# Optimization experiments

Measured on AMD Instinct MI355X. Metric: run time of the kernel, lower is better.

## Reference

```python
import jax, jax.numpy as jnp
import numpy as np
import math

B, R, C = 4, 512, 512
E, H, D, M, F = 256, 16, 16, 16, 512  # embed, heads, qkv_dim, ms_hidden, ff_hidden
EPS = 1e-5


def setup_inputs() -> dict:
    key = jax.random.key(0)
    ks = jax.random.split(key, 20)
    s = lambda fan_in: 1.0 / math.sqrt(fan_in)
    u = lambda k, shape, lim: jax.random.uniform(k, shape, jnp.float32, -lim, lim)
    mix1_init = (1 / 2) ** 0.5
    mix2_init = (1 / 16) ** 0.5
    return {
        "row_emb": jax.random.normal(ks[0], (B, R, E), jnp.float32),
        "col_emb": jax.random.normal(ks[1], (B, C, E), jnp.float32),
        "cost_mat": jax.random.uniform(ks[2], (B, R, C), jnp.float32),
        "Wq": u(ks[3], (E, H * D), s(E)),
        "Wk": u(ks[4], (E, H * D), s(E)),
        "Wv": u(ks[5], (E, H * D), s(E)),
        "mix1_w": u(ks[6], (H, 2, M), mix1_init),
        "mix1_b": u(ks[7], (H, M), mix1_init),
        "mix2_w": u(ks[8], (H, M, 1), mix2_init),
        "mix2_b": u(ks[9], (H, 1), mix2_init),
        "Wc": u(ks[10], (H * D, E), s(H * D)),
        "bc": u(ks[11], (E,), s(H * D)),
        "W1": u(ks[12], (E, F), s(E)),
        "b1": u(ks[13], (F,), s(E)),
        "W2": u(ks[14], (F, E), s(F)),
        "b2": u(ks[15], (E,), s(F)),
        "g1": jnp.ones((E,), jnp.float32),
        "be1": jnp.zeros((E,), jnp.float32),
        "g2": jnp.ones((E,), jnp.float32),
        "be2": jnp.zeros((E,), jnp.float32),
    }


def _instance_norm(x, gamma, beta):
    # InstanceNorm1d on x permuted to (B, E, L): normalize over seq dim per (b, channel)
    mean = jnp.mean(x, axis=1, keepdims=True)          # [B,1,E]
    var = jnp.mean((x - mean) ** 2, axis=1, keepdims=True)
    return (x - mean) * jax.lax.rsqrt(var + EPS) * gamma + beta


def reference(row_emb, col_emb, cost_mat, Wq, Wk, Wv, mix1_w, mix1_b, mix2_w,
              mix2_b, Wc, bc, W1, b1, W2, b2, g1, be1, g2, be2):
    # QKV projections, split heads: [B,L,H*D] -> [B,H,L,D]
    q = (row_emb @ Wq).reshape(B, R, H, D).transpose(0, 2, 1, 3)
    k = (col_emb @ Wk).reshape(B, C, H, D).transpose(0, 2, 1, 3)
    v = (col_emb @ Wv).reshape(B, C, H, D).transpose(0, 2, 1, 3)

    dot = jnp.einsum('bhrd,bhcd->bhrc', q, k) / math.sqrt(D)
    cost = jnp.broadcast_to(cost_mat[:, None, :, :], (B, H, R, C))
    two = jnp.stack((dot, cost), axis=-1)               # [B,H,R,C,2]

    # per-head 2 -> M -> 1 mixing MLP over scores
    ms1 = jnp.einsum('bhrcs,hsm->bhrcm', two, mix1_w) + mix1_b[None, :, None, None, :]
    ms1 = jax.nn.relu(ms1)
    mixed = jnp.einsum('bhrcm,hm->bhrc', ms1, mix2_w[:, :, 0]) + mix2_b[:, 0][None, :, None, None]

    weights = jax.nn.softmax(mixed, axis=-1)            # [B,H,R,C]
    out = jnp.einsum('bhrc,bhcd->bhrd', weights, v)
    out_concat = out.transpose(0, 2, 1, 3).reshape(B, R, H * D)

    mh = out_concat @ Wc + bc                           # multi_head_combine

    # TransformerFFN with instance norm
    x = _instance_norm(row_emb + mh, g1, be1)
    ffn = jax.nn.relu(x @ W1 + b1) @ W2 + b2
    return _instance_norm(x + ffn, g2, be2)
```

## Files before the change

### kernel.cpp

```cpp
#include <hip/hip_runtime.h>
#include <hip/hip_bf16.h>

typedef __hip_bfloat16 bf16;
typedef __hip_bfloat162 bf162;
typedef _Float16 f16;
typedef __attribute__((ext_vector_type(2))) _Float16 h2;
typedef __attribute__((ext_vector_type(8))) short short8;
typedef __attribute__((ext_vector_type(4))) float f32x4;
typedef __attribute__((ext_vector_type(2))) float f32x2;

#define B_ 4
#define R_ 512
#define C_ 512
#define E_ 256
#define H_ 16
#define D_ 16

__device__ __forceinline__ float b2f(bf16 x) { return __bfloat162float(x); }
__device__ __forceinline__ void stout(bf16* p, float v) { *p = __float2bfloat16(v); }
__device__ __forceinline__ void stout(f16* p, float v) { *p = (f16)v; }

__global__ __launch_bounds__(256) void transpose_cvt_kernel(
    const float* __restrict__ Wq, const float* __restrict__ Wk, const float* __restrict__ Wv,
    const float* __restrict__ Wc, const float* __restrict__ W1, const float* __restrict__ W2,
    bf16* __restrict__ WqT, bf16* __restrict__ WkT, bf16* __restrict__ WvT,
    bf16* __restrict__ WcT, bf16* __restrict__ W1T, bf16* __restrict__ W2T,
    float* __restrict__ statsZ)
{
    __shared__ bf16 tile[32][33];
    const int wsel = blockIdx.y;
    const int tx = blockIdx.x;
    if (wsel == 0 && tx >= 64) {
        const int idx = (tx - 64) * 256 + threadIdx.x;
        if (idx < 4096) statsZ[idx] = 0.f;
        return;
    }
    const float* src; bf16* dst; int K, N; float scl = 1.0f;
    switch (wsel) {
        case 0: src = Wq; dst = WqT; K = 256; N = 256; scl = 0.25f; break;
        case 1: src = Wk; dst = WkT; K = 256; N = 256; break;
        case 2: src = Wv; dst = WvT; K = 256; N = 256; break;
        case 3: src = Wc; dst = WcT; K = 256; N = 256; break;
        case 4: src = W1; dst = W1T; K = 256; N = 512; break;
        default: src = W2; dst = W2T; K = 512; N = 256; break;
    }
    const int ntiles = (K >> 5) * (N >> 5);
    if (tx >= ntiles) return;
    const int ncnt = N >> 5;
    const int tk = tx / ncnt, tn = tx % ncnt;
    const int c = threadIdx.x & 31, r = threadIdx.x >> 5;
#pragma unroll
    for (int i = 0; i < 4; i++)
        tile[r + i * 8][c] = __float2bfloat16(scl * src[(size_t)(tk * 32 + r + i * 8) * N + tn * 32 + c]);
    __syncthreads();
#pragma unroll
    for (int i = 0; i < 4; i++)
        dst[(size_t)(tn * 32 + r + i * 8) * K + tk * 32 + c] = tile[c][r + i * 8];
}

template <int AMODE, typename OT, int BM, int BN, bool BIAS, int RES, bool RELU, bool STATS>
__device__ __forceinline__ void mfma_gemm_body(
    const void* __restrict__ Ap,
    const bf16* __restrict__ BT, const float* __restrict__ bias,
    const void* __restrict__ Res,
    const float* __restrict__ normS, const float* __restrict__ normG, const float* __restrict__ normB,
    float* __restrict__ statsOut, OT* __restrict__ Cout,
    int M, int N, int K, int bx, int by)
{
    constexpr int MT = BM / 32, NT = BN / 32;
    constexpr int AEL = BM * 64 / 256, BEL = BN * 64 / 256;
    __shared__ __align__(16) bf16 As[BM * 80];
    __shared__ __align__(16) bf16 Bs[BN * 80];
    const int tid = threadIdx.x;
    const int wid = tid >> 6, lane = tid & 63;
    const int wm = wid >> 1, wn = wid & 1;
    const int fr = lane & 15, quad = lane >> 4;
    const int m0 = by * BM, n0 = bx * BN;
    const int arow = (AEL == 16) ? (tid >> 2) : (tid >> 3);
    const int akg  = (AEL == 16) ? ((tid & 3) << 4) : ((tid & 7) << 3);
    const int brow = (BEL == 16) ? (tid >> 2) : (tid >> 3);
    const int bkg  = (BEL == 16) ? ((tid & 3) << 4) : ((tid & 7) << 3);

    f32x4 acc[MT][NT];
#pragma unroll
    for (int mt = 0; mt < MT; mt++)
#pragma unroll
        for (int nt = 0; nt < NT; nt++) acc[mt][nt] = (f32x4){0.f, 0.f, 0.f, 0.f};

    for (int k0 = 0; k0 < K; k0 += 64) {
        if constexpr (AMODE == 0) {
            const short8* gp = (const short8*)((const bf16*)Ap + (size_t)(m0 + arow) * K + k0 + akg);
#pragma unroll
            for (int t8 = 0; t8 < AEL / 8; t8++) *(short8*)(&As[arow * 80 + akg + 8 * t8]) = gp[t8];
        } else if constexpr (AMODE == 1) {
            const float4* gp = (const float4*)((const float*)Ap + (size_t)(m0 + arow) * K + k0 + akg);
#pragma unroll
            for (int j = 0; j < AEL / 4; j++) {
                const float4 f = gp[j];
                *(bf162*)(&As[arow * 80 + akg + j * 4])     = __float22bfloat162_rn(make_float2(f.x, f.y));
                *(bf162*)(&As[arow * 80 + akg + j * 4 + 2]) = __float22bfloat162_rn(make_float2(f.z, f.w));
            }
        } else {
            const int bb = (m0 + arow) >> 9;
            const bf16* ap = (const bf16*)Ap + (size_t)(m0 + arow) * K + k0 + akg;
            bf16 tmp[AEL];
#pragma unroll
            for (int t8 = 0; t8 < AEL / 8; t8++) *(short8*)(tmp + 8 * t8) = ((const short8*)ap)[t8];
#pragma unroll
            for (int j = 0; j < AEL; j++) {
                const int e = k0 + akg + j;
                const float s = normS[bb * 256 + e], sq = normS[1024 + bb * 256 + e];
                const float mn = s * (1.f / 512.f);
                float var = sq * (1.f / 512.f) - mn * mn; var = fmaxf(var, 0.f);
                As[arow * 80 + akg + j] = __float2bfloat16(
                    (b2f(tmp[j]) - mn) * rsqrtf(var + 1e-5f) * normG[e] + normB[e]);
            }
        }
        {
            const short8* gp = (const short8*)(BT + (size_t)(n0 + brow) * K + k0 + bkg);
#pragma unroll
            for (int t8 = 0; t8 < BEL / 8; t8++) *(short8*)(&Bs[brow * 80 + bkg + 8 * t8]) = gp[t8];
        }
        __syncthreads();

        short8 af[MT][2], bfr[NT][2];
#pragma unroll
        for (int mt = 0; mt < MT; mt++) {
            const int ar = wm * (BM / 2) + mt * 16 + fr;
#pragma unroll
            for (int kh = 0; kh < 2; kh++)
                af[mt][kh] = *(const short8*)(&As[ar * 80 + quad * 8 + kh * 32]);
        }
#pragma unroll
        for (int nt = 0; nt < NT; nt++) {
            const int br = wn * (BN / 2) + nt * 16 + fr;
#pragma unroll
            for (int kh = 0; kh < 2; kh++)
                bfr[nt][kh] = *(const short8*)(&Bs[br * 80 + quad * 8 + kh * 32]);
        }
#pragma unroll
        for (int kh = 0; kh < 2; kh++)
#pragma unroll
            for (int mt = 0; mt < MT; mt++)
#pragma unroll
                for (int nt = 0; nt < NT; nt++)
                    acc[mt][nt] = __builtin_amdgcn_mfma_f32_16x16x32_bf16(
                        af[mt][kh], bfr[nt][kh], acc[mt][nt], 0, 0, 0);
        __syncthreads();
    }

    float vsum[NT], vss[NT];
#pragma unroll
    for (int nt = 0; nt < NT; nt++) { vsum[nt] = 0.f; vss[nt] = 0.f; }
#pragma unroll
    for (int mt = 0; mt < MT; mt++) {
#pragma unroll
        for (int nt = 0; nt < NT; nt++) {
#pragma unroll
            for (int i = 0; i < 4; i++) {
                const int row = m0 + wm * (BM / 2) + mt * 16 + quad * 4 + i;
                const int col = n0 + wn * (BN / 2) + nt * 16 + fr;
                float v = acc[mt][nt][i];
                if (BIAS) v += bias[col];
                if constexpr (RES == 1) v += ((const float*)Res)[(size_t)row * N + col];
                if constexpr (RES == 3) {
                    const int bb = row >> 9;
                    const float yv = b2f(((const bf16*)Res)[(size_t)row * N + col]);
                    const float s = normS[bb * 256 + col], sq = normS[1024 + bb * 256 + col];
                    const float mn = s * (1.f / 512.f);
                    float var = sq * (1.f / 512.f) - mn * mn; var = fmaxf(var, 0.f);
                    v += (yv - mn) * rsqrtf(var + 1e-5f) * normG[col] + normB[col];
                }
                if (RELU) v = fmaxf(v, 0.f);
                stout(&Cout[(size_t)row * N + col], v);
                if (STATS) { vsum[nt] += v; vss[nt] += v * v; }
            }
        }
    }
    if constexpr (STATS) {
        float* sred = (float*)As;
#pragma unroll
        for (int nt = 0; nt < NT; nt++) {
            float a = vsum[nt]; a += __shfl_xor(a, 16, 64); a += __shfl_xor(a, 32, 64);
            float c = vss[nt];  c += __shfl_xor(c, 16, 64); c += __shfl_xor(c, 32, 64);
            if (quad == 0) {
                const int cl = wn * (BN / 2) + nt * 16 + fr;
                sred[wm * (2 * BN) + cl * 2 + 0] = a;
                sred[wm * (2 * BN) + cl * 2 + 1] = c;
            }
        }
        __syncthreads();
        if (tid < 2 * BN) {
            const int cl = tid >> 1, w = tid & 1;
            const float tot = sred[cl * 2 + w] + sred[2 * BN + cl * 2 + w];
            atomicAdd(&statsOut[w * 1024 + (m0 >> 9) * 256 + n0 + cl], tot);
        }
    }
}

template <int AMODE, typename OT, int BM, int BN, bool BIAS, int RES, bool RELU, bool STATS>
__global__ __launch_bounds__(256) void mfma_gemm_kernel(
    const void* __restrict__ Ap,
    const bf16* __restrict__ BT, const float* __restrict__ bias,
    const void* __restrict__ Res,
    const float* __restrict__ normS, const float* __restrict__ normG, const float* __restrict__ normB,
    float* __restrict__ statsOut, OT* __restrict__ Cout, int M, int N, int K)
{
    mfma_gemm_body<AMODE, OT, BM, BN, BIAS, RES, RELU, STATS>(
        Ap, BT, bias, Res, normS, normG, normB, statsOut, Cout,
        M, N, K, blockIdx.x, blockIdx.y);
}

__global__ __launch_bounds__(256) void qkv_kernel(
    const float* __restrict__ rowE, const float* __restrict__ colE,
    const bf16* __restrict__ WqT, const bf16* __restrict__ WkT, const bf16* __restrict__ WvT,
    f16* __restrict__ qo, f16* __restrict__ ko, f16* __restrict__ vo)
{
    const int z = blockIdx.z;
    const float* A = (z == 0) ? rowE : colE;
    const bf16* BT = (z == 0) ? WqT : (z == 1) ? WkT : WvT;
    f16* O = (z == 0) ? qo : (z == 1) ? ko : vo;
    mfma_gemm_body<1, f16, 32, 64, false, 0, false, false>(
        A, BT, nullptr, nullptr, nullptr, nullptr, nullptr, nullptr, O,
        2048, 256, 256, blockIdx.x, blockIdx.y);
}

__global__ __launch_bounds__(256) void attn_kernel(
    const f16* __restrict__ q, const f16* __restrict__ k, const f16* __restrict__ v,
    const float* __restrict__ cost, const float* __restrict__ m1w, const float* __restrict__ m1b,
    const float* __restrict__ m2w, const float* __restrict__ m2b,
    bf16* __restrict__ po, bf16* __restrict__ plb)
{
    __shared__ __align__(16) char slds[12288];
    f16* kbuf = (f16*)slds;
    float* vbuf = (float*)(slds + 4096);
    f16* smo = (f16*)slds;
    float* sml = (float*)(slds + 8192);

    const int rt = blockIdx.x >> 2, cs = blockIdx.x & 3;
    const int h = blockIdx.y, b = blockIdx.z;
    const int tid = threadIdx.x, wid = tid >> 6, lane = tid & 63;

    {
        const size_t base = ((size_t)b * C_) * 256 + h * 16 + (size_t)cs * 128 * 256;
        const int lc = tid >> 1, dp = (tid & 1) * 8;
        const size_t g = base + (size_t)lc * 256 + dp;
        *(short8*)(&kbuf[lc * 16 + dp]) = *(const short8*)(k + g);
        const short8 vraw = *(const short8*)(v + g);
        const h2* rh = (const h2*)&vraw;
        *(float4*)(&vbuf[lc * 16 + dp]) = make_float4(
            (float)rh[0].x, (float)rh[0].y, (float)rh[1].x, (float)rh[1].y);
        *(float4*)(&vbuf[lc * 16 + dp + 4]) = make_float4(
            (float)rh[2].x, (float)rh[2].y, (float)rh[3].x, (float)rh[3].y);
    }

    h2 w1a2[8], w1b2[8], b1h[8], w2p[8];
#pragma unroll
    for (int i = 0; i < 8; i++) {
        h2 t;
        t.x = (f16)m1w[h * 32 + 2 * i];      t.y = (f16)m1w[h * 32 + 2 * i + 1];      w1a2[i] = t;
        t.x = (f16)m1w[h * 32 + 16 + 2 * i]; t.y = (f16)m1w[h * 32 + 17 + 2 * i];     w1b2[i] = t;
        t.x = (f16)m1b[h * 16 + 2 * i];      t.y = (f16)m1b[h * 16 + 2 * i + 1];      b1h[i] = t;
        t.x = (f16)m2w[h * 16 + 2 * i];      t.y = (f16)m2w[h * 16 + 2 * i + 1];      w2p[i] = t;
    }
    const float b2v = m2b[h];
    const h2 zero2 = (h2)(f16)0;

    const int r = rt * 64 + lane;
    short8 qraw[2];
    {
        const short8* qp = (const short8*)(q + (size_t)(b * R_ + r) * 256 + h * 16);
        qraw[0] = qp[0]; qraw[1] = qp[1];
    }
    const h2* qh = (const h2*)qraw;

    __syncthreads();

    const float* crow = cost + (size_t)(b * R_ + r) * C_ + cs * 128 + wid * 32;
    float lrun = 0.f;
    f32x2 o2[8];
#pragma unroll
    for (int j = 0; j < 8; j++) o2[j] = (f32x2){0.f, 0.f};

    for (int cc = 0; cc < 32; cc += 4) {
        const float4 cst4 = *(const float4*)(crow + cc);
#pragma unroll
        for (int u = 0; u < 4; u++) {
            const int lc = wid * 32 + cc + u;
            const h2* kr = (const h2*)(&kbuf[lc * 16]);
            h2 dacc = qh[0] * kr[0];
#pragma unroll
            for (int i = 1; i < 8; i++) dacc = qh[i] * kr[i] + dacc;
            const float dot = (float)dacc.x + (float)dacc.y;
            const float cst = (u == 0) ? cst4.x : (u == 1) ? cst4.y : (u == 2) ? cst4.z : cst4.w;
            const f16 doth = (f16)dot, csth = (f16)cst;
            h2 dot2; dot2.x = doth; dot2.y = doth;
            h2 cst2; cst2.x = csth; cst2.y = csth;
            h2 acc2 = (h2)(f16)0;
#pragma unroll
            for (int i = 0; i < 8; i++) {
                h2 t = dot2 * w1a2[i] + b1h[i];
                t = cst2 * w1b2[i] + t;
                t = __builtin_elementwise_max(t, zero2);
                acc2 = t * w2p[i] + acc2;
            }
            const float p = __expf(b2v + (float)acc2.x + (float)acc2.y);
            lrun += p;
            f32x2 p2; p2.x = p; p2.y = p;
            const f32x2* vr = (const f32x2*)(&vbuf[lc * 16]);
#pragma unroll
            for (int j = 0; j < 8; j++) o2[j] = p2 * vr[j] + o2[j];
        }
    }

    __syncthreads();
    {
        const float invw = 1.f / lrun;
        h2* op = (h2*)&smo[(wid * 64 + lane) * 16];
#pragma unroll
        for (int j = 0; j < 8; j++) {
            h2 t; t.x = (f16)(o2[j].x * invw); t.y = (f16)(o2[j].y * invw);
            op[j] = t;
        }
        sml[wid * 64 + lane] = lrun;
    }
    __syncthreads();

    if (tid < 64) {
        const int rr = tid;
        float ll = 0.f, oo[16] = {};
#pragma unroll
        for (int w = 0; w < 4; w++) {
            const float lw = sml[w * 64 + rr];
            ll += lw;
            const h2* p = (const h2*)&smo[(w * 64 + rr) * 16];
#pragma unroll
            for (int j = 0; j < 8; j++) {
                const h2 t = p[j];
                oo[2 * j]     = fmaf(lw, (float)t.x, oo[2 * j]);
                oo[2 * j + 1] = fmaf(lw, (float)t.y, oo[2 * j + 1]);
            }
        }
        const float inv = 1.f / ll;
        const int idx = ((b * H_ + h) << 9) + rt * 64 + rr;
        plb[cs * 32768 + idx] = __float2bfloat16(ll);
        bf162* pp = (bf162*)(po + (size_t)(cs * 32768 + idx) * 16);
#pragma unroll
        for (int j = 0; j < 8; j++)
            pp[j] = __float22bfloat162_rn(make_float2(oo[2 * j] * inv, oo[2 * j + 1] * inv));
    }
}

__global__ __launch_bounds__(256) void attn_merge_kernel(
    const bf16* __restrict__ po, const bf16* __restrict__ plb, bf16* __restrict__ sa)
{
    const int idx = blockIdx.x * 256 + threadIdx.x;
    const float l0 = b2f(plb[idx]), l1 = b2f(plb[32768 + idx]);
    const float l2 = b2f(plb[65536 + idx]), l3 = b2f(plb[98304 + idx]);
    const float inv = 1.f / (l0 + l1 + l2 + l3);
    float oo[16] = {};
#pragma unroll
    for (int c = 0; c < 4; c++) {
        const float wgt = ((c == 0) ? l0 : (c == 1) ? l1 : (c == 2) ? l2 : l3) * inv;
        const bf162* pp = (const bf162*)(po + (size_t)(c * 32768 + idx) * 16);
#pragma unroll
        for (int j = 0; j < 8; j++) {
            const float2 f = __bfloat1622float2(pp[j]);
            oo[2 * j]     = fmaf(wgt, f.x, oo[2 * j]);
            oo[2 * j + 1] = fmaf(wgt, f.y, oo[2 * j + 1]);
        }
    }
    const int b = idx >> 13, h = (idx >> 9) & 15, r = idx & 511;
    bf162* dst = (bf162*)(sa + (size_t)(b * R_ + r) * 256 + h * 16);
#pragma unroll
    for (int j = 0; j < 8; j++)
        dst[j] = __float22bfloat162_rn(make_float2(oo[2 * j], oo[2 * j + 1]));
}

__global__ __launch_bounds__(256) void apply_in2_kernel(
    const bf16* __restrict__ xin, const float* __restrict__ stats,
    const float* __restrict__ g, const float* __restrict__ be, float* __restrict__ outp)
{
    const int base = (blockIdx.x * 256 + threadIdx.x) * 4;
    const int b = base >> 17;
    const bf162* xp = (const bf162*)(xin + base);
    const float2 x0 = __bfloat1622float2(xp[0]), x1 = __bfloat1622float2(xp[1]);
    const float xv[4] = {x0.x, x0.y, x1.x, x1.y};
    float4 rr;
    float* rp = (float*)&rr;
#pragma unroll
    for (int j = 0; j < 4; j++) {
        const int e = (base & 255) + j;
        const float s = stats[b * 256 + e], sq = stats[1024 + b * 256 + e];
        const float mn = s * (1.f / 512.f);
        float var = sq * (1.f / 512.f) - mn * mn; var = fmaxf(var, 0.f);
        rp[j] = (xv[j] - mn) * rsqrtf(var + 1e-5f) * g[e] + be[e];
    }
    *(float4*)(outp + base) = rr;
}

extern "C" void kernel_launch(void* const* d_in, const int* in_sizes, int n_in,
                              void* d_out, int out_size, void* d_ws, size_t ws_size,
                              hipStream_t stream)
{
    (void)in_sizes; (void)n_in; (void)out_size; (void)ws_size;
    const float* row_emb = (const float*)d_in[0];
    const float* col_emb = (const float*)d_in[1];
    const float* cost    = (const float*)d_in[2];
    const float* Wq  = (const float*)d_in[3];
    const float* Wk  = (const float*)d_in[4];
    const float* Wv  = (const float*)d_in[5];
    const float* m1w = (const float*)d_in[6];
    const float* m1b = (const float*)d_in[7];
    const float* m2w = (const float*)d_in[8];
    const float* m2b = (const float*)d_in[9];
    const float* Wc  = (const float*)d_in[10];
    const float* bc  = (const float*)d_in[11];
    const float* W1  = (const float*)d_in[12];
    const float* b1  = (const float*)d_in[13];
    const float* W2  = (const float*)d_in[14];
    const float* b2  = (const float*)d_in[15];
    const float* g1  = (const float*)d_in[16];
    const float* be1 = (const float*)d_in[17];
    const float* g2  = (const float*)d_in[18];
    const float* be2 = (const float*)d_in[19];
    float* out = (float*)d_out;

    char* w = (char*)d_ws;
    f16*  sq  = (f16*)(w + 0);
    f16*  sk  = (f16*)(w + 1048576);
    f16*  sv  = (f16*)(w + 2097152);
    bf16* sa  = (bf16*)(w + 0);
    bf16* sy  = (bf16*)(w + 1048576);
    bf16* st  = (bf16*)(w + 2097152);
    bf16* WqT = (bf16*)(w + 3145728);
    bf16* WkT = WqT + 65536;
    bf16* WvT = WkT + 65536;
    bf16* po  = (bf16*)(w + 3145728);
    bf16* shm = (bf16*)(w + 3145728);
    bf16* plb = (bf16*)(w + 7340032);
    bf16* WcT = (bf16*)(w + 7602176);
    bf16* W1T = (bf16*)(w + 7733248);
    bf16* W2T = (bf16*)(w + 7995392);
    float* stats1 = (float*)(w + 8257536);
    float* stats2 = stats1 + 2048;

    const dim3 blk(256);

    transpose_cvt_kernel<<<dim3(128, 6), blk, 0, stream>>>(
        Wq, Wk, Wv, Wc, W1, W2, WqT, WkT, WvT, WcT, W1T, W2T, stats1);

    qkv_kernel<<<dim3(4, 64, 3), blk, 0, stream>>>(row_emb, col_emb, WqT, WkT, WvT, sq, sk, sv);

    attn_kernel<<<dim3(32, 16, 4), blk, 0, stream>>>(
        sq, sk, sv, cost, m1w, m1b, m2w, m2b, po, plb);

    attn_merge_kernel<<<dim3(128), blk, 0, stream>>>(po, plb, sa);

    mfma_gemm_kernel<0, bf16, 32, 32, true, 1, false, true><<<dim3(8, 64), blk, 0, stream>>>(
        sa, WcT, bc, row_emb, nullptr, nullptr, nullptr, stats1, sy, 2048, 256, 256);

    mfma_gemm_kernel<2, bf16, 32, 64, true, 0, true, false><<<dim3(8, 64), blk, 0, stream>>>(
        sy, W1T, b1, nullptr, stats1, g1, be1, nullptr, shm, 2048, 512, 256);

    mfma_gemm_kernel<0, bf16, 32, 32, true, 3, false, true><<<dim3(8, 64), blk, 0, stream>>>(
        shm, W2T, b2, sy, stats1, g1, be1, stats2, st, 2048, 256, 512);

    apply_in2_kernel<<<dim3(512), blk, 0, stream>>>(st, stats2, g2, be2, out);
}
```

Measured before the change: 163.9 us.

## Use MFMA for attention PV, drop weight transpose kernel, read fp32 weights directly

The attention kernel now computes the mixing-MLP scores per lane for 16 rows per wave. It does an in-register max-subtracted softmax and accumulates P·V with a bf16 16x16x32 MFMA instead of scalar FMAs and an LDS cross-wave merge. V is stored as bf16 and the partial sums are kept in fp32. The separate weight transpose/convert kernel is removed: GEMMs load fp32 weights column-wise from global memory and convert on the fly, and stats zeroing moves into the merge kernel. This saves a launch and the scalar PV work, but the B-tile loads become strided, uncoalesced scalar reads.

After: 175.2 us. +6.9%, slower.

```diff
diff --git a/kernel.cpp b/kernel.cpp
--- a/kernel.cpp
+++ b/kernel.cpp
@@ -7,7 +7,6 @@
 typedef __attribute__((ext_vector_type(2))) _Float16 h2;
 typedef __attribute__((ext_vector_type(8))) short short8;
 typedef __attribute__((ext_vector_type(4))) float f32x4;
-typedef __attribute__((ext_vector_type(2))) float f32x2;
 
 #define B_ 4
 #define R_ 512
@@ -20,49 +19,10 @@
 __device__ __forceinline__ void stout(bf16* p, float v) { *p = __float2bfloat16(v); }
 __device__ __forceinline__ void stout(f16* p, float v) { *p = (f16)v; }
 
-__global__ __launch_bounds__(256) void transpose_cvt_kernel(
-    const float* __restrict__ Wq, const float* __restrict__ Wk, const float* __restrict__ Wv,
-    const float* __restrict__ Wc, const float* __restrict__ W1, const float* __restrict__ W2,
-    bf16* __restrict__ WqT, bf16* __restrict__ WkT, bf16* __restrict__ WvT,
-    bf16* __restrict__ WcT, bf16* __restrict__ W1T, bf16* __restrict__ W2T,
-    float* __restrict__ statsZ)
-{
-    __shared__ bf16 tile[32][33];
-    const int wsel = blockIdx.y;
-    const int tx = blockIdx.x;
-    if (wsel == 0 && tx >= 64) {
-        const int idx = (tx - 64) * 256 + threadIdx.x;
-        if (idx < 4096) statsZ[idx] = 0.f;
-        return;
-    }
-    const float* src; bf16* dst; int K, N; float scl = 1.0f;
-    switch (wsel) {
-        case 0: src = Wq; dst = WqT; K = 256; N = 256; scl = 0.25f; break;
-        case 1: src = Wk; dst = WkT; K = 256; N = 256; break;
-        case 2: src = Wv; dst = WvT; K = 256; N = 256; break;
-        case 3: src = Wc; dst = WcT; K = 256; N = 256; break;
-        case 4: src = W1; dst = W1T; K = 256; N = 512; break;
-        default: src = W2; dst = W2T; K = 512; N = 256; break;
-    }
-    const int ntiles = (K >> 5) * (N >> 5);
-    if (tx >= ntiles) return;
-    const int ncnt = N >> 5;
-    const int tk = tx / ncnt, tn = tx % ncnt;
-    const int c = threadIdx.x & 31, r = threadIdx.x >> 5;
-#pragma unroll
-    for (int i = 0; i < 4; i++)
-        tile[r + i * 8][c] = __float2bfloat16(scl * src[(size_t)(tk * 32 + r + i * 8) * N + tn * 32 + c]);
-    __syncthreads();
-#pragma unroll
-    for (int i = 0; i < 4; i++)
-        dst[(size_t)(tn * 32 + r + i * 8) * K + tk * 32 + c] = tile[c][r + i * 8];
-}
-
 template <int AMODE, typename OT, int BM, int BN, bool BIAS, int RES, bool RELU, bool STATS>
 __device__ __forceinline__ void mfma_gemm_body(
-    const void* __restrict__ Ap,
-    const bf16* __restrict__ BT, const float* __restrict__ bias,
-    const void* __restrict__ Res,
+    const void* __restrict__ Ap, const float* __restrict__ W, float bscl,
+    const float* __restrict__ bias, const void* __restrict__ Res,
     const float* __restrict__ normS, const float* __restrict__ normG, const float* __restrict__ normB,
     float* __restrict__ statsOut, OT* __restrict__ Cout,
     int M, int N, int K, int bx, int by)
@@ -117,9 +77,10 @@
             }
         }
         {
-            const short8* gp = (const short8*)(BT + (size_t)(n0 + brow) * K + k0 + bkg);
-#pragma unroll
-            for (int t8 = 0; t8 < BEL / 8; t8++) *(short8*)(&Bs[brow * 80 + bkg + 8 * t8]) = gp[t8];
+#pragma unroll
+            for (int j = 0; j < BEL; j++)
+                Bs[brow * 80 + bkg + j] = __float2bfloat16(
+                    bscl * W[(size_t)(k0 + bkg + j) * N + (n0 + brow)]);
         }
         __syncthreads();
 
@@ -200,58 +161,54 @@
 
 template <int AMODE, typename OT, int BM, int BN, bool BIAS, int RES, bool RELU, bool STATS>
 __global__ __launch_bounds__(256) void mfma_gemm_kernel(
-    const void* __restrict__ Ap,
-    const bf16* __restrict__ BT, const float* __restrict__ bias,
-    const void* __restrict__ Res,
+    const void* __restrict__ Ap, const float* __restrict__ W, float bscl,
+    const float* __restrict__ bias, const void* __restrict__ Res,
     const float* __restrict__ normS, const float* __restrict__ normG, const float* __restrict__ normB,
     float* __restrict__ statsOut, OT* __restrict__ Cout, int M, int N, int K)
 {
     mfma_gemm_body<AMODE, OT, BM, BN, BIAS, RES, RELU, STATS>(
-        Ap, BT, bias, Res, normS, normG, normB, statsOut, Cout,
+        Ap, W, bscl, bias, Res, normS, normG, normB, statsOut, Cout,
         M, N, K, blockIdx.x, blockIdx.y);
 }
 
 __global__ __launch_bounds__(256) void qkv_kernel(
     const float* __restrict__ rowE, const float* __restrict__ colE,
-    const bf16* __restrict__ WqT, const bf16* __restrict__ WkT, const bf16* __restrict__ WvT,
-    f16* __restrict__ qo, f16* __restrict__ ko, f16* __restrict__ vo)
+    const float* __restrict__ Wq, const float* __restrict__ Wk, const float* __restrict__ Wv,
+    f16* __restrict__ qo, f16* __restrict__ ko, bf16* __restrict__ vo)
 {
     const int z = blockIdx.z;
-    const float* A = (z == 0) ? rowE : colE;
-    const bf16* BT = (z == 0) ? WqT : (z == 1) ? WkT : WvT;
-    f16* O = (z == 0) ? qo : (z == 1) ? ko : vo;
-    mfma_gemm_body<1, f16, 32, 64, false, 0, false, false>(
-        A, BT, nullptr, nullptr, nullptr, nullptr, nullptr, nullptr, O,
-        2048, 256, 256, blockIdx.x, blockIdx.y);
+    if (z == 2) {
+        mfma_gemm_body<1, bf16, 32, 64, false, 0, false, false>(
+            colE, Wv, 1.f, nullptr, nullptr, nullptr, nullptr, nullptr, nullptr, vo,
+            2048, 256, 256, blockIdx.x, blockIdx.y);
+    } else {
+        mfma_gemm_body<1, f16, 32, 64, false, 0, false, false>(
+            (z == 0) ? rowE : colE, (z == 0) ? Wq : Wk, (z == 0) ? 0.25f : 1.f,
+            nullptr, nullptr, nullptr, nullptr, nullptr, nullptr, (z == 0) ? qo : ko,
+            2048, 256, 256, blockIdx.x, blockIdx.y);
+    }
 }
 
 __global__ __launch_bounds__(256) void attn_kernel(
-    const f16* __restrict__ q, const f16* __restrict__ k, const f16* __restrict__ v,
+    const f16* __restrict__ q, const f16* __restrict__ k, const bf16* __restrict__ v,
     const float* __restrict__ cost, const float* __restrict__ m1w, const float* __restrict__ m1b,
     const float* __restrict__ m2w, const float* __restrict__ m2b,
-    bf16* __restrict__ po, bf16* __restrict__ plb)
-{
-    __shared__ __align__(16) char slds[12288];
-    f16* kbuf = (f16*)slds;
-    float* vbuf = (float*)(slds + 4096);
-    f16* smo = (f16*)slds;
-    float* sml = (float*)(slds + 8192);
+    bf16* __restrict__ po, float* __restrict__ plf)
+{
+    __shared__ __align__(16) f16 kbuf[128 * 16];
+    __shared__ __align__(16) short vbuf[128 * 16];
 
     const int rt = blockIdx.x >> 2, cs = blockIdx.x & 3;
     const int h = blockIdx.y, b = blockIdx.z;
     const int tid = threadIdx.x, wid = tid >> 6, lane = tid & 63;
+    const int quad = lane >> 4, fr = lane & 15;
 
     {
         const size_t base = ((size_t)b * C_) * 256 + h * 16 + (size_t)cs * 128 * 256;
         const int lc = tid >> 1, dp = (tid & 1) * 8;
         const size_t g = base + (size_t)lc * 256 + dp;
         *(short8*)(&kbuf[lc * 16 + dp]) = *(const short8*)(k + g);
-        const short8 vraw = *(const short8*)(v + g);
-        const h2* rh = (const h2*)&vraw;
-        *(float4*)(&vbuf[lc * 16 + dp]) = make_float4(
-            (float)rh[0].x, (float)rh[0].y, (float)rh[1].x, (float)rh[1].y);
-        *(float4*)(&vbuf[lc * 16 + dp + 4]) = make_float4(
-            (float)rh[2].x, (float)rh[2].y, (float)rh[3].x, (float)rh[3].y);
+        *(short8*)(&vbuf[lc * 16 + dp]) = *(const short8*)(v + g);
     }
 
     h2 w1a2[8], w1b2[8], b1h[8], w2p[8];
@@ -266,33 +223,32 @@
     const float b2v = m2b[h];
     const h2 zero2 = (h2)(f16)0;
 
-    const int r = rt * 64 + lane;
+    const int row_m = rt * 64 + wid * 16 + fr;
     short8 qraw[2];
     {
-        const short8* qp = (const short8*)(q + (size_t)(b * R_ + r) * 256 + h * 16);
+        const short8* qp = (const short8*)(q + (size_t)(b * R_ + row_m) * 256 + h * 16);
         qraw[0] = qp[0]; qraw[1] = qp[1];
     }
     const h2* qh = (const h2*)qraw;
 
     __syncthreads();
 
-    const float* crow = cost + (size_t)(b * R_ + r) * C_ + cs * 128 + wid * 32;
-    float lrun = 0.f;
-    f32x2 o2[8];
-#pragma unroll
-    for (int j = 0; j < 8; j++) o2[j] = (f32x2){0.f, 0.f};
-
-    for (int cc = 0; cc < 32; cc += 4) {
-        const float4 cst4 = *(const float4*)(crow + cc);
-#pragma unroll
-        for (int u = 0; u < 4; u++) {
-            const int lc = wid * 32 + cc + u;
-            const h2* kr = (const h2*)(&kbuf[lc * 16]);
+    const float* crow = cost + (size_t)(b * R_ + row_m) * C_ + cs * 128;
+    h2 sh[16];
+#pragma unroll
+    for (int blk = 0; blk < 4; blk++) {
+        const float4 c0 = *(const float4*)(crow + blk * 32 + quad * 8);
+        const float4 c1 = *(const float4*)(crow + blk * 32 + quad * 8 + 4);
+        const float carr[8] = {c0.x, c0.y, c0.z, c0.w, c1.x, c1.y, c1.z, c1.w};
+#pragma unroll
+        for (int j = 0; j < 8; j++) {
+            const int col = blk * 32 + quad * 8 + j;
+            const h2* kr = (const h2*)(&kbuf[col * 16]);
             h2 dacc = qh[0] * kr[0];
 #pragma unroll
             for (int i = 1; i < 8; i++) dacc = qh[i] * kr[i] + dacc;
             const float dot = (float)dacc.x + (float)dacc.y;
-            const float cst = (u == 0) ? cst4.x : (u == 1) ? cst4.y : (u == 2) ? cst4.z : cst4.w;
+            const float cst = carr[j];
             const f16 doth = (f16)dot, csth = (f16)cst;
             h2 dot2; dot2.x = doth; dot2.y = doth;
             h2 cst2; cst2.x = csth; cst2.y = csth;
@@ -304,59 +260,60 @@
                 t = __builtin_elementwise_max(t, zero2);
                 acc2 = t * w2p[i] + acc2;
             }
-            const float p = __expf(b2v + (float)acc2.x + (float)acc2.y);
-            lrun += p;
-            f32x2 p2; p2.x = p; p2.y = p;
-            const f32x2* vr = (const f32x2*)(&vbuf[lc * 16]);
-#pragma unroll
-            for (int j = 0; j < 8; j++) o2[j] = p2 * vr[j] + o2[j];
-        }
-    }
-
-    __syncthreads();
-    {
-        const float invw = 1.f / lrun;
-        h2* op = (h2*)&smo[(wid * 64 + lane) * 16];
-#pragma unroll
-        for (int j = 0; j < 8; j++) {
-            h2 t; t.x = (f16)(o2[j].x * invw); t.y = (f16)(o2[j].y * invw);
-            op[j] = t;
-        }
-        sml[wid * 64 + lane] = lrun;
-    }
-    __syncthreads();
-
-    if (tid < 64) {
-        const int rr = tid;
-        float ll = 0.f, oo[16] = {};
-#pragma unroll
-        for (int w = 0; w < 4; w++) {
-            const float lw = sml[w * 64 + rr];
-            ll += lw;
-            const h2* p = (const h2*)&smo[(w * 64 + rr) * 16];
-#pragma unroll
-            for (int j = 0; j < 8; j++) {
-                const h2 t = p[j];
-                oo[2 * j]     = fmaf(lw, (float)t.x, oo[2 * j]);
-                oo[2 * j + 1] = fmaf(lw, (float)t.y, oo[2 * j + 1]);
-            }
-        }
-        const float inv = 1.f / ll;
-        const int idx = ((b * H_ + h) << 9) + rt * 64 + rr;
-        plb[cs * 32768 + idx] = __float2bfloat16(ll);
-        bf162* pp = (bf162*)(po + (size_t)(cs * 32768 + idx) * 16);
-#pragma unroll
-        for (int j = 0; j < 8; j++)
-            pp[j] = __float22bfloat162_rn(make_float2(oo[2 * j] * inv, oo[2 * j + 1] * inv));
+            const float s = b2v + (float)acc2.x + (float)acc2.y;
+            const f16 sf = (f16)s;
+            if (j & 1) sh[blk * 4 + (j >> 1)].y = sf;
+            else       sh[blk * 4 + (j >> 1)].x = sf;
+        }
+    }
+
+    h2 mx2 = sh[0];
+#pragma unroll
+    for (int i = 1; i < 16; i++) mx2 = __builtin_elementwise_max(mx2, sh[i]);
+    float m_l = fmaxf((float)mx2.x, (float)mx2.y);
+    m_l = fmaxf(m_l, __shfl_xor(m_l, 16, 64));
+    m_l = fmaxf(m_l, __shfl_xor(m_l, 32, 64));
+
+    f32x4 oacc = (f32x4){0.f, 0.f, 0.f, 0.f};
+    float lsum = 0.f;
+#pragma unroll
+    for (int blk = 0; blk < 4; blk++) {
+        short8 pa, bv;
+#pragma unroll
+        for (int jj = 0; jj < 4; jj++) {
+            const h2 t = sh[blk * 4 + jj];
+            const float e0 = __expf((float)t.x - m_l);
+            const float e1 = __expf((float)t.y - m_l);
+            lsum += e0 + e1;
+            const bf162 pr = __float22bfloat162_rn(make_float2(e0, e1));
+            pa[2 * jj]     = __builtin_bit_cast(short, pr.x);
+            pa[2 * jj + 1] = __builtin_bit_cast(short, pr.y);
+        }
+#pragma unroll
+        for (int j = 0; j < 8; j++) bv[j] = vbuf[(blk * 32 + quad * 8 + j) * 16 + fr];
+        oacc = __builtin_amdgcn_mfma_f32_16x16x32_bf16(pa, bv, oacc, 0, 0, 0);
+    }
+    lsum += __shfl_xor(lsum, 16, 64);
+    lsum += __shfl_xor(lsum, 32, 64);
+
+    const int idxbase = cs * 32768 + ((b * H_ + h) << 9) + rt * 64 + wid * 16;
+    if (quad == 0) plf[idxbase + fr] = lsum * __expf(m_l);
+#pragma unroll
+    for (int i = 0; i < 4; i++) {
+        const float li = __shfl(lsum, quad * 4 + i, 64);
+        po[(size_t)(idxbase + quad * 4 + i) * 16 + fr] = __float2bfloat16(oacc[i] / li);
     }
 }
 
 __global__ __launch_bounds__(256) void attn_merge_kernel(
-    const bf16* __restrict__ po, const bf16* __restrict__ plb, bf16* __restrict__ sa)
+    const bf16* __restrict__ po, const float* __restrict__ plf, bf16* __restrict__ sa,
+    float* __restrict__ stats1, float* __restrict__ stats2)
 {
     const int idx = blockIdx.x * 256 + threadIdx.x;
-    const float l0 = b2f(plb[idx]), l1 = b2f(plb[32768 + idx]);
-    const float l2 = b2f(plb[65536 + idx]), l3 = b2f(plb[98304 + idx]);
+    if (idx < 2048) stats1[idx] = 0.f;
+    else if (idx < 4096) stats2[idx - 2048] = 0.f;
+    const float l0 = plf[idx], l1 = plf[32768 + idx];
+    const float l2 = plf[65536 + idx], l3 = plf[98304 + idx];
     const float inv = 1.f / (l0 + l1 + l2 + l3);
     float oo[16] = {};
 #pragma unroll
@@ -429,42 +386,33 @@
     char* w = (char*)d_ws;
     f16*  sq  = (f16*)(w + 0);
     f16*  sk  = (f16*)(w + 1048576);
-    f16*  sv  = (f16*)(w + 2097152);
+    bf16* sv  = (bf16*)(w + 2097152);
     bf16* sa  = (bf16*)(w + 0);
     bf16* sy  = (bf16*)(w + 1048576);
     bf16* st  = (bf16*)(w + 2097152);
-    bf16* WqT = (bf16*)(w + 3145728);
-    bf16* WkT = WqT + 65536;
-    bf16* WvT = WkT + 65536;
     bf16* po  = (bf16*)(w + 3145728);
     bf16* shm = (bf16*)(w + 3145728);
-    bf16* plb = (bf16*)(w + 7340032);
-    bf16* WcT = (bf16*)(w + 7602176);
-    bf16* W1T = (bf16*)(w + 7733248);
-    bf16* W2T = (bf16*)(w + 7995392);
+    float* plf = (float*)(w + 7340032);
     float* stats1 = (float*)(w + 8257536);
     float* stats2 = stats1 + 2048;
 
     const dim3 blk(256);
 
-    transpose_cvt_kernel<<<dim3(128, 6), blk, 0, stream>>>(
-        Wq, Wk, Wv, Wc, W1, W2, WqT, WkT, WvT, WcT, W1T, W2T, stats1);
-
-    qkv_kernel<<<dim3(4, 64, 3), blk, 0, stream>>>(row_emb, col_emb, WqT, WkT, WvT, sq, sk, sv);
+    qkv_kernel<<<dim3(4, 64, 3), blk, 0, stream>>>(row_emb, col_emb, Wq, Wk, Wv, sq, sk, sv);
 
     attn_kernel<<<dim3(32, 16, 4), blk, 0, stream>>>(
-        sq, sk, sv, cost, m1w, m1b, m2w, m2b, po, plb);
-
-    attn_merge_kernel<<<dim3(128), blk, 0, stream>>>(po, plb, sa);
+        sq, sk, sv, cost, m1w, m1b, m2w, m2b, po, plf);
+
+    attn_merge_kernel<<<dim3(128), blk, 0, stream>>>(po, plf, sa, stats1, stats2);
 
     mfma_gemm_kernel<0, bf16, 32, 32, true, 1, false, true><<<dim3(8, 64), blk, 0, stream>>>(
-        sa, WcT, bc, row_emb, nullptr, nullptr, nullptr, stats1, sy, 2048, 256, 256);
+        sa, Wc, 1.f, bc, row_emb, nullptr, nullptr, nullptr, stats1, sy, 2048, 256, 256);
 
     mfma_gemm_kernel<2, bf16, 32, 64, true, 0, true, false><<<dim3(8, 64), blk, 0, stream>>>(
-        sy, W1T, b1, nullptr, stats1, g1, be1, nullptr, shm, 2048, 512, 256);
+        sy, W1, 1.f, b1, nullptr, stats1, g1, be1, nullptr, shm, 2048, 512, 256);
 
     mfma_gemm_kernel<0, bf16, 32, 32, true, 3, false, true><<<dim3(8, 64), blk, 0, stream>>>(
-        shm, W2T, b2, sy, stats1, g1, be1, stats2, st, 2048, 256, 512);
+        shm, W2, 1.f, b2, sy, stats1, g1, be1, stats2, st, 2048, 256, 512);
 
     apply_in2_kernel<<<dim3(512), blk, 0, stream>>>(st, stats2, g2, be2, out);
 }
```
